# Kernel optimization log

Measured on AMD Instinct MI355X. Metric: run time of the kernel, lower is better.

The kernel has to match this reference:

```python
import jax, jax.numpy as jnp
import numpy as np

P = 16                     # patch size
D = 192                    # embed dim (forced by SAT d_model=192)
NHEAD = 3                  # ViT-Tiny heads
SAT_H, SAT_DK, SAT_DV = 8, 32, 32
N_SLICE = 10
PER_LI = jnp.linspace(0.1, 1.0, N_SLICE)
LN_EPS = 1e-5


def layernorm(z, g, b):
    m = z.mean(-1, keepdims=True)
    v = ((z - m) ** 2).mean(-1, keepdims=True)
    return (z - m) * jax.lax.rsqrt(v + LN_EPS) * g + b


def setup_inputs() -> dict:
    key = jax.random.key(0)
    ks = jax.random.split(key, 32)
    B, IMG, DEPTH, MLP = 128, 224, 12, 4 * D
    S = (IMG // P) ** 2 + 1  # 197 tokens
    n = lambda k, sh: jax.random.normal(k, sh, jnp.float32) * 0.02
    z = lambda sh: jnp.zeros(sh, jnp.float32)
    o = lambda sh: jnp.ones(sh, jnp.float32)
    return {
        "x": jax.random.uniform(ks[0], (B, 3, IMG, IMG), jnp.float32),
        "x_g_norm": jax.random.uniform(ks[1], (B, 1, 56, 56), jnp.float32),
        "patch_w": n(ks[2], (D, 3, P, P)), "patch_b": z((D,)),
        "cls_token": n(ks[3], (1, 1, D)), "pos_embed": n(ks[4], (1, S, D)),
        "eleva_embed": n(ks[5], (1, D)),
        "sat_wq": n(ks[6], (D, SAT_H * SAT_DK)), "sat_bq": z((SAT_H * SAT_DK,)),
        "sat_wk": n(ks[7], (D, SAT_H * SAT_DK)), "sat_bk": z((SAT_H * SAT_DK,)),
        "sat_wv": n(ks[8], (D, SAT_H * SAT_DV)), "sat_bv": z((SAT_H * SAT_DV,)),
        "sat_wo": n(ks[9], (SAT_H * SAT_DV, D)), "sat_bo": z((D,)),
        "ln1_g": o((DEPTH, D)), "ln1_b": z((DEPTH, D)),
        "qkv_w": n(ks[10], (DEPTH, D, 3 * D)), "qkv_b": z((DEPTH, 3 * D)),
        "proj_w": n(ks[11], (DEPTH, D, D)), "proj_b": z((DEPTH, D)),
        "ln2_g": o((DEPTH, D)), "ln2_b": z((DEPTH, D)),
        "fc1_w": n(ks[12], (DEPTH, D, MLP)), "fc1_b": z((DEPTH, MLP)),
        "fc2_w": n(ks[13], (DEPTH, MLP, D)), "fc2_b": z((DEPTH, D)),
        "norm_g": o((D,)), "norm_b": z((D,)),
    }


def _forward(x, x_g_norm, patch_w, patch_b, cls_token, pos_embed, eleva_embed,
             sat_wq, sat_bq, sat_wk, sat_bk, sat_wv, sat_bv, sat_wo, sat_bo,
             ln1_g, ln1_b, qkv_w, qkv_b, proj_w, proj_b, ln2_g, ln2_b,
             fc1_w, fc1_b, fc2_w, fc2_b, norm_g, norm_b):
    B = x.shape[0]
    # --- patch embed: Conv2d(3, D, kernel=P, stride=P) -> [B, N, D] ---
    feat = jax.lax.conv_general_dilated(
        x, patch_w, (P, P), 'VALID', dimension_numbers=('NCHW', 'OIHW', 'NCHW'))
    feat = feat + patch_b[None, :, None, None]
    tokens = feat.reshape(B, D, -1).transpose(0, 2, 1)          # [B, 196, D]
    tok = jnp.concatenate([jnp.broadcast_to(cls_token, (B, 1, D)), tokens], axis=1)
    tok = tok + pos_embed                                        # [B, S, D]
    S = tok.shape[1]
    # --- elevation weight per sample (vectorized bisect + linear interp) ---
    means = x_g_norm.mean(axis=(1, 2, 3))                        # [B]
    idx = jnp.clip(jnp.searchsorted(PER_LI, means, side='left'), 0, N_SLICE - 1)
    per_hi = PER_LI[idx]
    per_lo = jnp.where(idx == 0, 0.0, PER_LI[jnp.maximum(idx - 1, 0)])
    idx_f = idx.astype(jnp.float32)
    idx_inter = idx_f - (per_hi - means) / (per_hi - per_lo)
    w = jnp.where(idx == N_SLICE - 1, idx_f, idx_inter) / N_SLICE  # [B]
    # --- SAT fusion: per (batch, token) a 2-element attention over (token, ele) ---
    ele = jnp.broadcast_to(eleva_embed[0] * w[:, None, None], tok.shape)  # [B,S,D]
    at_in = jnp.stack([tok, ele], axis=2)                        # [B, S, 2, D]
    q = (at_in @ sat_wq + sat_bq).reshape(B, S, 2, SAT_H, SAT_DK)
    k = (at_in @ sat_wk + sat_bk).reshape(B, S, 2, SAT_H, SAT_DK)
    v = (at_in @ sat_wv + sat_bv).reshape(B, S, 2, SAT_H, SAT_DV)
    att = jnp.einsum('bsqhd,bskhd->bshqk', q, k) * (1.0 / np.sqrt(SAT_DK))
    att = jax.nn.softmax(att, axis=-1)
    sat_o = jnp.einsum('bshqk,bskhd->bsqhd', att, v).reshape(B, S, 2, SAT_H * SAT_DV)
    sat_o = sat_o @ sat_wo + sat_bo                              # [B, S, 2, D]
    h = sat_o[..., 0, :] + sat_o[..., 1, :]                      # [B, S, D]
    # --- ViT blocks via scan over stacked layer params ---
    hd = D // NHEAD

    def block(z, p):
        l1g, l1b, qw, qb, pw, pb, l2g, l2b, f1w, f1b, f2w, f2b = p
        y = layernorm(z, l1g, l1b)
        qkv = y @ qw + qb                                        # [B, S, 3D]
        q_, k_, v_ = jnp.split(qkv, 3, axis=-1)
        q_ = q_.reshape(B, S, NHEAD, hd)
        k_ = k_.reshape(B, S, NHEAD, hd)
        v_ = v_.reshape(B, S, NHEAD, hd)
        a = jnp.einsum('bqhd,bkhd->bhqk', q_, k_) * (hd ** -0.5)
        a = jax.nn.softmax(a, axis=-1)
        o = jnp.einsum('bhqk,bkhd->bqhd', a, v_).reshape(B, S, D)
        z = z + o @ pw + pb
        y = layernorm(z, l2g, l2b)
        z = z + jax.nn.gelu(y @ f1w + f1b, approximate=False) @ f2w + f2b
        return z, None

    h, _ = jax.lax.scan(block, h, (ln1_g, ln1_b, qkv_w, qkv_b, proj_w, proj_b,
                                   ln2_g, ln2_b, fc1_w, fc1_b, fc2_w, fc2_b))
    h = layernorm(h, norm_g, norm_b)
    return h[:, 0]                                               # [B, D] cls token


def reference(x, x_g_norm, patch_w, patch_b, cls_token, pos_embed, eleva_embed,
              sat_wq, sat_bq, sat_wk, sat_bk, sat_wv, sat_bv, sat_wo, sat_bo,
              ln1_g, ln1_b, qkv_w, qkv_b, proj_w, proj_b, ln2_g, ln2_b,
              fc1_w, fc1_b, fc2_w, fc2_b, norm_g, norm_b):
    return _forward(x, x_g_norm, patch_w, patch_b, cls_token, pos_embed, eleva_embed,
                    sat_wq, sat_bq, sat_wk, sat_bk, sat_wv, sat_bv, sat_wo, sat_bo,
                    ln1_g, ln1_b, qkv_w, qkv_b, proj_w, proj_b, ln2_g, ln2_b,
                    fc1_w, fc1_b, fc2_w, fc2_b, norm_g, norm_b)
```

## Files before the change

### kernel.cpp

```cpp
#include <hip/hip_runtime.h>


#define BATCH 128
#define SEQ 197
#define BS_ROWS (BATCH * SEQ)
#define DMODEL 192
#define NPATCH 196
#define MROWS_PATCH (BATCH * NPATCH)
#define KPATCH 768
#define MLPDIM 768
#define DEPTH 12
#define SPAD 224

typedef float f32x4 __attribute__((ext_vector_type(4)));
typedef short s16x8 __attribute__((ext_vector_type(8)));

#define AS1 __attribute__((address_space(1)))
#define AS3 __attribute__((address_space(3)))

__device__ __forceinline__ float wredSum(float v) {
#pragma unroll
  for (int o = 32; o > 0; o >>= 1) v += __shfl_xor(v, o, 64);
  return v;
}

__device__ __forceinline__ unsigned short f2bf(float f) {
  union { float f; unsigned u; } v;
  v.f = f;
  unsigned r = v.u + 0x7FFFu + ((v.u >> 16) & 1u);
  return (unsigned short)(r >> 16);
}
__device__ __forceinline__ float bf2f(unsigned short u) {
  union { unsigned u; float f; } v;
  v.u = ((unsigned)u) << 16;
  return v.f;
}

__device__ __forceinline__ int swz(int col, int row) {
  int g8 = col >> 3;
  g8 = (g8 & ~7) | ((g8 & 7) ^ (row & 7));
  return (g8 << 3) | (col & 7);
}

__device__ __forceinline__ float gelu(float x) {
  const float ax = fabsf(x) * 0.70710678118654752f;
  const float t = 1.f / (1.f + 0.3275911f * ax);
  const float y =
      t * (0.254829592f +
           t * (-0.284496736f +
                t * (1.421413741f + t * (-1.453152027f + t * 1.061405429f))));
  const float erfc_ = y * __expf(-ax * ax);
  const float cdf = (x >= 0.f) ? (1.f - 0.5f * erfc_) : (0.5f * erfc_);
  return x * cdf;
}

__global__ __launch_bounds__(256) void eleva_w_kernel(const float* __restrict__ xg,
                                                      float* __restrict__ wout) {
  const int b = blockIdx.x;
  const float* p = xg + (size_t)b * 3136;
  float s = 0.f;
  for (int i = threadIdx.x; i < 3136; i += 256) s += p[i];
  __shared__ float partial[4];
  s = wredSum(s);
  if ((threadIdx.x & 63) == 0) partial[threadIdx.x >> 6] = s;
  __syncthreads();
  if (threadIdx.x == 0) {
    float m = (partial[0] + partial[1] + partial[2] + partial[3]) / 3136.f;
    int idx = 0;
#pragma unroll
    for (int i = 0; i < 10; i++) {
      float pv = 0.1f * (float)(i + 1);
      if (pv < m) idx = i + 1;
    }
    if (idx > 9) idx = 9;
    float wv;
    if (idx == 9) {
      wv = 9.f;
    } else {
      float hi = 0.1f * (float)(idx + 1);
      float lo = (idx == 0) ? 0.f : 0.1f * (float)idx;
      wv = (float)idx - (hi - m) / (hi - lo);
    }
    wout[b] = wv / 10.f;
  }
}

__global__ __launch_bounds__(256) void wprep_kernel(
    const float* __restrict__ qkv_w, const float* __restrict__ proj_w,
    const float* __restrict__ fc1_w, const float* __restrict__ fc2_w,
    const float* __restrict__ satq, const float* __restrict__ satk,
    const float* __restrict__ satv, const float* __restrict__ sato,
    unsigned short* __restrict__ qkv_wt, unsigned short* __restrict__ proj_wt,
    unsigned short* __restrict__ fc1_wt, unsigned short* __restrict__ fc2_wt,
    unsigned short* __restrict__ satqkv_t, unsigned short* __restrict__ sato_t) {
  int bid = blockIdx.x;
  const float* in;
  unsigned short* out;
  int R, C;
  if (bid < 1296) {
    in = qkv_w; out = qkv_wt; R = 192; C = 576;
  } else if ((bid -= 1296) < 432) {
    in = proj_w; out = proj_wt; R = 192; C = 192;
  } else if ((bid -= 432) < 1728) {
    in = fc1_w; out = fc1_wt; R = 192; C = 768;
  } else if ((bid -= 1728) < 1728) {
    in = fc2_w; out = fc2_wt; R = 768; C = 192;
  } else if ((bid -= 1728) < 48) {
    in = satq; out = satqkv_t; R = 192; C = 256;
  } else if ((bid -= 48) < 48) {
    in = satk; out = satqkv_t + 49152; R = 192; C = 256;
  } else if ((bid -= 48) < 48) {
    in = satv; out = satqkv_t + 98304; R = 192; C = 256;
  } else {
    bid -= 48;
    in = sato; out = sato_t; R = 256; C = 192;
  }
  const int tilesX = C >> 5;
  const int tpm = (R >> 5) * tilesX;
  const int mat = bid / tpm;
  const int t_ = bid - mat * tpm;
  const int ty = t_ / tilesX, tx = t_ - ty * tilesX;
  in += (size_t)mat * R * C;
  out += (size_t)mat * R * C;
  const int c0 = tx * 32, r0 = ty * 32;
  __shared__ float t[32][33];
  const int tr = threadIdx.x >> 3, tc = (threadIdx.x & 7) * 4;
  const float4 v = *(const float4*)(in + (size_t)(r0 + tr) * C + c0 + tc);
  t[tr][tc] = v.x; t[tr][tc + 1] = v.y; t[tr][tc + 2] = v.z; t[tr][tc + 3] = v.w;
  __syncthreads();
  ushort4 o;
  o.x = f2bf(t[tc + 0][tr]);
  o.y = f2bf(t[tc + 1][tr]);
  o.z = f2bf(t[tc + 2][tr]);
  o.w = f2bf(t[tc + 3][tr]);
  const int brow = c0 + tr;
  *(ushort4*)(out + (size_t)brow * R + swz(r0 + tc, brow)) = o;
}

__global__ __launch_bounds__(256) void convert_kernel(const float* __restrict__ in,
                                                      unsigned short* __restrict__ out, int n4,
                                                      int K) {
  const int i = blockIdx.x * 256 + threadIdx.x;
  if (i >= n4) return;
  const int flat = i * 4;
  const int row = flat / K, col = flat % K;
  const float4 v = *(const float4*)(in + flat);
  ushort4 o;
  o.x = f2bf(v.x); o.y = f2bf(v.y); o.z = f2bf(v.z); o.w = f2bf(v.w);
  *(ushort4*)(out + (size_t)row * K + swz(col, row)) = o;
}

__global__ __launch_bounds__(256) void im2col_kernel(const float* __restrict__ x,
                                                     unsigned short* __restrict__ col) {
  const int i = blockIdx.x * 256 + threadIdx.x;
  if (i >= MROWS_PATCH * KPATCH / 8) return;
  const int k = (i % 96) * 8, row = i / 96;
  const int b = row / NPATCH, p = row % NPATCH;
  const int py = p / 14, px = p % 14;
  const int c = k >> 8, r = (k >> 4) & 15, cc = k & 15;
  const float* src = x + (((size_t)b * 3 + c) * 224 + (py * 16 + r)) * 224 + (px * 16 + cc);
  const float4 v0 = *(const float4*)src;
  const float4 v1 = *(const float4*)(src + 4);
  s16x8 o;
  o[0] = (short)f2bf(v0.x); o[1] = (short)f2bf(v0.y);
  o[2] = (short)f2bf(v0.z); o[3] = (short)f2bf(v0.w);
  o[4] = (short)f2bf(v1.x); o[5] = (short)f2bf(v1.y);
  o[6] = (short)f2bf(v1.z); o[7] = (short)f2bf(v1.w);
  *(s16x8*)(col + (size_t)row * KPATCH + swz(k, row)) = o;
}

__global__ __launch_bounds__(256) void cls_kernel(const float* __restrict__ cls,
                                                  const float* __restrict__ pos,
                                                  float* __restrict__ H,
                                                  unsigned short* __restrict__ Hbf) {
  const int i = blockIdx.x * 256 + threadIdx.x;
  if (i >= BATCH * DMODEL) return;
  const int b = i / DMODEL, d = i % DMODEL;
  const float v = cls[d] + pos[d];
  const int row = b * SEQ;
  H[(size_t)row * DMODEL + d] = v;
  Hbf[(size_t)row * DMODEL + swz(d, row)] = f2bf(v);
}

__global__ __launch_bounds__(256) void ele_proj_kernel(
    const float* __restrict__ ele_emb, const float* __restrict__ wq, const float* __restrict__ bq,
    const float* __restrict__ wk, const float* __restrict__ bk,
    const float* __restrict__ wv, const float* __restrict__ bv,
    const float* __restrict__ wvec, float* __restrict__ eq, float* __restrict__ ek,
    float* __restrict__ ev, float* __restrict__ satb) {
  const int b = blockIdx.x, t = threadIdx.x;
  if (b == 0) {
    satb[t] = bq[t];
    satb[256 + t] = bk[t];
    satb[512 + t] = bv[t];
  }
  __shared__ float es[DMODEL];
  if (t < DMODEL) es[t] = ele_emb[t] * wvec[b];
  __syncthreads();
  float aq = bq[t], ak = bk[t], av = bv[t];
  for (int d = 0; d < DMODEL; d++) {
    const float e = es[d];
    aq += e * wq[d * 256 + t];
    ak += e * wk[d * 256 + t];
    av += e * wv[d * 256 + t];
  }
  eq[b * 256 + t] = aq;
  ek[b * 256 + t] = ak;
  ev[b * 256 + t] = av;
}

__global__ __launch_bounds__(256) void sat_mix_kernel(
    const unsigned short* __restrict__ qkv768, const float* __restrict__ eq,
    const float* __restrict__ ek, const float* __restrict__ ev,
    unsigned short* __restrict__ o256) {
  const int gid = blockIdx.x * 256 + threadIdx.x;
  const int tok = gid >> 3, h = gid & 7;
  if (tok >= BS_ROWS) return;
  const int b = tok / SEQ;
  const unsigned short* qp = qkv768 + (size_t)tok * 768 + h * 32;
  s16x8 qv[4], kv[4];
#pragma unroll
  for (int i0 = 0; i0 < 4; i0++) {
    qv[i0] = *(const s16x8*)(qp + i0 * 8);
    kv[i0] = *(const s16x8*)(qp + 256 + i0 * 8);
  }
  float eqa[32], eka[32];
  {
    const float4* eqp = (const float4*)(eq + b * 256 + h * 32);
    const float4* ekp = (const float4*)(ek + b * 256 + h * 32);
#pragma unroll
    for (int i0 = 0; i0 < 8; i0++) {
      const float4 a = eqp[i0], c = ekp[i0];
      eqa[i0 * 4] = a.x; eqa[i0 * 4 + 1] = a.y; eqa[i0 * 4 + 2] = a.z; eqa[i0 * 4 + 3] = a.w;
      eka[i0 * 4] = c.x; eka[i0 * 4 + 1] = c.y; eka[i0 * 4 + 2] = c.z; eka[i0 * 4 + 3] = c.w;
    }
  }
  float s00 = 0.f, s01 = 0.f, s10 = 0.f, s11 = 0.f;
#pragma unroll
  for (int d = 0; d < 32; d++) {
    const float q_ = bf2f((unsigned short)qv[d >> 3][d & 7]);
    const float k_ = bf2f((unsigned short)kv[d >> 3][d & 7]);
    s00 += q_ * k_;
    s01 += q_ * eka[d];
    s10 += eqa[d] * k_;
    s11 += eqa[d] * eka[d];
  }
  const float sc = 0.17677669529663687f;
  s00 *= sc; s01 *= sc; s10 *= sc; s11 *= sc;
  const float m0 = fmaxf(s00, s01), m1 = fmaxf(s10, s11);
  const float e00 = __expf(s00 - m0), e01 = __expf(s01 - m0);
  const float e10 = __expf(s10 - m1), e11 = __expf(s11 - m1);
  const float w0 = e00 / (e00 + e01) + e10 / (e10 + e11);
  const float w1 = e01 / (e00 + e01) + e11 / (e10 + e11);
  unsigned short* op = o256 + (size_t)tok * 256;
  const float4* evp = (const float4*)(ev + b * 256 + h * 32);
#pragma unroll
  for (int i0 = 0; i0 < 4; i0++) {
    const s16x8 vv = *(const s16x8*)(qp + 512 + i0 * 8);
    const float4 e0 = evp[i0 * 2], e1 = evp[i0 * 2 + 1];
    float ev8[8] = {e0.x, e0.y, e0.z, e0.w, e1.x, e1.y, e1.z, e1.w};
    s16x8 o;
#pragma unroll
    for (int e = 0; e < 8; e++)
      o[e] = (short)f2bf(w0 * bf2f((unsigned short)vv[e]) + w1 * ev8[e]);
    *(s16x8*)(op + swz(h * 32 + i0 * 8, tok)) = o;
  }
}

template <int EPI, bool SWZO, int BN, int BM>
__global__ __launch_bounds__(256, 4)
void gemm_mfma(const unsigned short* __restrict__ A,
               const unsigned short* __restrict__ Bt,
               const float* __restrict__ bias,
               const float* __restrict__ res,
               void* __restrict__ Cout,
               unsigned short* __restrict__ aux_hbf,
               const float* __restrict__ aux_pos,
               const float* __restrict__ lng,
               const float* __restrict__ lnb,
               int M, int N, int K, int nx) {
  constexpr int NJ = 3;
  constexpr int MI = (BM == 128) ? 4 : 2;
  constexpr bool LNF = (EPI == 5 || EPI == 6);
  constexpr int LNROWS = LNF ? BM : 1;
  int mt, nt;
  if (BM == 128) {
    const int bid = blockIdx.x;
    const int e = bid & 7, i = bid >> 3;
    nt = i % nx;
    mt = e + 8 * (i / nx);
    if (mt * BM >= M) return;
  } else {
    mt = blockIdx.y;
    nt = blockIdx.x;
  }
  __shared__ unsigned short As[BM * 64];
  __shared__ unsigned short Bs[BN * 64];
  __shared__ float2 lnbuf[4][LNROWS];
  const int tid = threadIdx.x, lane = tid & 63, w = tid >> 6;
  const int n0 = nt * BN;
  const int m0 = mt * BM;
  const int c = lane & 15, g = lane >> 4;
  const int wm = (BM == 128) ? (w >> 1) * 64 : 0;
  const int wn = (BM == 128) ? (w & 1) * 96 / 2 : w * 48;
  f32x4 acc[MI][NJ] = {};

  const int ar = (lane >> 3);
  const int acol = (lane & 7) * 8;

  for (int k0 = 0; k0 < K; k0 += 64) {
#pragma unroll
    for (int it = 0; it < BM / 32; it++) {
      const int r = w * (BM / 4) + it * 8 + ar;
      const unsigned short* gp = A + (size_t)(m0 + r) * K + k0 + acol;
      __builtin_amdgcn_global_load_lds(
          (const AS1 unsigned int*)gp,
          (AS3 unsigned int*)(As + (w * (BM / 4) + it * 8) * 64), 16, 0, 0);
    }
#pragma unroll
    for (int it = 0; it < BN / 32; it++) {
      const int r = w * (BN / 4) + it * 8 + ar;
      const unsigned short* gp = Bt + (size_t)(n0 + r) * K + k0 + acol;
      __builtin_amdgcn_global_load_lds(
          (const AS1 unsigned int*)gp,
          (AS3 unsigned int*)(Bs + (w * (BN / 4) + it * 8) * 64), 16, 0, 0);
    }
    __syncthreads();
#pragma unroll
    for (int kk = 0; kk < 2; kk++) {
      const int sw = (((kk * 4 + g) ^ (c & 7))) << 3;
      s16x8 af[MI], bfr[NJ];
#pragma unroll
      for (int i = 0; i < MI; i++)
        af[i] = *(const s16x8*)&As[(wm + i * 16 + c) * 64 + sw];
#pragma unroll
      for (int j = 0; j < NJ; j++)
        bfr[j] = *(const s16x8*)&Bs[(wn + j * 16 + c) * 64 + sw];
#pragma unroll
      for (int i = 0; i < MI; i++)
#pragma unroll
        for (int j = 0; j < NJ; j++)
          acc[i][j] = __builtin_amdgcn_mfma_f32_16x16x32_bf16(af[i], bfr[j], acc[i][j], 0, 0, 0);
    }
    __syncthreads();
  }

  const int ncol0 = n0 + wn + c;
  float bv[NJ];
#pragma unroll
  for (int j = 0; j < NJ; j++) bv[j] = bias[ncol0 + j * 16] * (EPI == 6 ? 2.f : 1.f);

  if constexpr (LNF) {
#pragma unroll
    for (int i = 0; i < MI; i++) {
#pragma unroll
      for (int r_ = 0; r_ < 4; r_++) {
        const int lr = wm + i * 16 + g * 4 + r_;
        const int mrow = m0 + lr;
        float s1 = 0.f, s2 = 0.f;
#pragma unroll
        for (int j = 0; j < NJ; j++) {
          float v = acc[i][j][r_] + bv[j];
          if (EPI == 5) v += res[(size_t)mrow * DMODEL + ncol0 + j * 16];
          acc[i][j][r_] = v;
          ((float*)Cout)[(size_t)mrow * DMODEL + ncol0 + j * 16] = v;
          s1 += v;
          s2 += v * v;
        }
#pragma unroll
        for (int o = 1; o <= 8; o <<= 1) {
          s1 += __shfl_xor(s1, o, 64);
          s2 += __shfl_xor(s2, o, 64);
        }
        if (c == 0) lnbuf[w][lr] = make_float2(s1, s2);
      }
    }
    __syncthreads();
    float lg[NJ], lb[NJ];
#pragma unroll
    for (int j = 0; j < NJ; j++) { lg[j] = lng[ncol0 + j * 16]; lb[j] = lnb[ncol0 + j * 16]; }
#pragma unroll
    for (int i = 0; i < MI; i++) {
#pragma unroll
      for (int r_ = 0; r_ < 4; r_++) {
        const int lr = wm + i * 16 + g * 4 + r_;
        const int mrow = m0 + lr;
        const float2 a0 = lnbuf[0][lr], a1 = lnbuf[1][lr];
        const float2 a2 = lnbuf[2][lr], a3 = lnbuf[3][lr];
        const float mean = (a0.x + a1.x + a2.x + a3.x) * (1.f / 192.f);
        const float var = (a0.y + a1.y + a2.y + a3.y) * (1.f / 192.f) - mean * mean;
        const float inv = rsqrtf(var + 1e-5f);
#pragma unroll
        for (int j = 0; j < NJ; j++) {
          const int col = ncol0 + j * 16;
          const float yn = (acc[i][j][r_] - mean) * inv * lg[j] + lb[j];
          aux_hbf[(size_t)mrow * DMODEL + swz(col, mrow)] = f2bf(yn);
        }
      }
    }
  } else if (EPI == 7 && n0 >= 384) {
#pragma unroll
    for (int i = 0; i < MI; i++) {
#pragma unroll
      for (int r_ = 0; r_ < 4; r_++) {
        const int mrow = m0 + wm + i * 16 + g * 4 + r_;
        const int b = mrow / SEQ;
        const int s = mrow - b * SEQ;
#pragma unroll
        for (int j = 0; j < NJ; j++) {
          const int vcol = ncol0 + j * 16 - 384;
          const int h = vcol >> 6, d = vcol & 63;
          aux_hbf[((size_t)((b * 3 + h) * 64 + d)) * SPAD + s] = f2bf(acc[i][j][r_] + bv[j]);
        }
      }
    }
  } else {
#pragma unroll
    for (int i = 0; i < MI; i++) {
#pragma unroll
      for (int r_ = 0; r_ < 4; r_++) {
        const int mrow = m0 + wm + i * 16 + g * 4 + r_;
        if (EPI == 4) {
          const int bb = mrow / 196;
          const int p = mrow - bb * 196;
          const int drow = mrow + bb + 1;
#pragma unroll
          for (int j = 0; j < NJ; j++) {
            const int col = ncol0 + j * 16;
            const float v = acc[i][j][r_] + bv[j] + aux_pos[(size_t)(p + 1) * DMODEL + col];
            ((float*)Cout)[(size_t)drow * DMODEL + col] = v;
            aux_hbf[(size_t)drow * DMODEL + swz(col, drow)] = f2bf(v);
          }
        } else {
#pragma unroll
          for (int j = 0; j < NJ; j++) {
            float v = acc[i][j][r_] + bv[j];
            const int col = ncol0 + j * 16;
            const size_t rowoff = (size_t)mrow * N;
            ((unsigned short*)Cout)[rowoff + (SWZO ? swz(col, mrow) : col)] = f2bf(v);
          }
        }
      }
    }
  }
}

__global__ __launch_bounds__(256, 2)
void mlp_fused_kernel(const unsigned short* __restrict__ Yin,
                      const unsigned short* __restrict__ w1,
                      const unsigned short* __restrict__ w2,
                      const float* __restrict__ b1,
                      const float* __restrict__ b2,
                      float* __restrict__ H,
                      unsigned short* __restrict__ Yout,
                      const float* __restrict__ lng,
                      const float* __restrict__ lnb) {
  __shared__ unsigned short Abuf[32 * 192];
  __shared__ unsigned short W1buf[64 * 192];
  __shared__ unsigned short W2buf[192 * 64];
  __shared__ unsigned short Pbuf[2][32 * 64];
  __shared__ float2 lnbuf[4][32];
  const int tid = threadIdx.x, lane = tid & 63, w = tid >> 6;
  const int c = lane & 15, g = lane >> 4;
  const int m0 = blockIdx.x * 32;

#pragma unroll
  for (int it = 0; it < 3; it++) {
    const int flat = w * 192 + it * 64 + lane;
    const int r = flat / 24, s = flat - r * 24;
    const unsigned short* gp = Yin + (size_t)(m0 + r) * DMODEL + s * 8;
    __builtin_amdgcn_global_load_lds((const AS1 unsigned int*)gp,
                                     (AS3 unsigned int*)(Abuf + flat * 8), 16, 0, 0);
  }
  auto stageW1 = [&](int ch) {
#pragma unroll
    for (int it = 0; it < 6; it++) {
      const int flat = w * 384 + it * 64 + lane;
      const int r = flat / 24, s = flat - r * 24;
      const unsigned short* gp = w1 + (size_t)(ch * 64 + r) * DMODEL + s * 8;
      __builtin_amdgcn_global_load_lds((const AS1 unsigned int*)gp,
                                       (AS3 unsigned int*)(W1buf + flat * 8), 16, 0, 0);
    }
  };
  auto stageW2 = [&](int ch) {
#pragma unroll
    for (int it = 0; it < 6; it++) {
      const int flat = w * 384 + it * 64 + lane;
      const int r = flat >> 3, s = flat & 7;
      const unsigned short* gp = w2 + (size_t)r * MLPDIM + ch * 64 + s * 8;
      __builtin_amdgcn_global_load_lds((const AS1 unsigned int*)gp,
                                       (AS3 unsigned int*)(W2buf + flat * 8), 16, 0, 0);
    }
  };
  stageW1(0);
  stageW2(0);
  __syncthreads();

  f32x4 acc2[2][3] = {};
  for (int ch = 0; ch < 12; ++ch) {
    const float bb1 = b1[ch * 64 + w * 16 + c];
    f32x4 a1[2] = {};
#pragma unroll
    for (int kk = 0; kk < 6; kk++) {
      const int slot = kk * 4 + g;
      const int sw1 = ((slot & ~7) | ((slot & 7) ^ (c & 7))) << 3;
      const s16x8 bf1 = *(const s16x8*)&W1buf[(w * 16 + c) * DMODEL + sw1];
#pragma unroll
      for (int i = 0; i < 2; i++) {
        const s16x8 af = *(const s16x8*)&Abuf[(i * 16 + c) * DMODEL + sw1];
        a1[i] = __builtin_amdgcn_mfma_f32_16x16x32_bf16(af, bf1, a1[i], 0, 0, 0);
      }
    }
    unsigned short* P = &Pbuf[ch & 1][0];
#pragma unroll
    for (int i = 0; i < 2; i++) {
#pragma unroll
      for (int r_ = 0; r_ < 4; r_++) {
        const int row = i * 16 + g * 4 + r_;
        const int col = w * 16 + c;
        const int slotp = (col >> 3) ^ (row & 7);
        P[row * 64 + slotp * 8 + (col & 7)] = f2bf(gelu(a1[i][r_] + bb1));
      }
    }
    __syncthreads();
    if (ch < 11) stageW1(ch + 1);
#pragma unroll
    for (int kk = 0; kk < 2; kk++) {
      const int slot = kk * 4 + g;
      const int sw2 = (slot ^ (c & 7)) << 3;
      s16x8 af2[2], bf2[3];
#pragma unroll
      for (int i = 0; i < 2; i++) af2[i] = *(const s16x8*)&P[(i * 16 + c) * 64 + sw2];
#pragma unroll
      for (int j = 0; j < 3; j++)
        bf2[j] = *(const s16x8*)&W2buf[(w * 48 + j * 16 + c) * 64 + sw2];
#pragma unroll
      for (int i = 0; i < 2; i++)
#pragma unroll
        for (int j = 0; j < 3; j++)
          acc2[i][j] = __builtin_amdgcn_mfma_f32_16x16x32_bf16(af2[i], bf2[j], acc2[i][j], 0, 0, 0);
    }
    __syncthreads();
    if (ch < 11) stageW2(ch + 1);
  }

  const int ncol0 = w * 48 + c;
  float bv[3];
#pragma unroll
  for (int j = 0; j < 3; j++) bv[j] = b2[ncol0 + j * 16];
#pragma unroll
  for (int i = 0; i < 2; i++) {
#pragma unroll
    for (int r_ = 0; r_ < 4; r_++) {
      const int lr = i * 16 + g * 4 + r_;
      const int mrow = m0 + lr;
      float s1 = 0.f, s2 = 0.f;
#pragma unroll
      for (int j = 0; j < 3; j++) {
        float v = acc2[i][j][r_] + bv[j] + H[(size_t)mrow * DMODEL + ncol0 + j * 16];
        acc2[i][j][r_] = v;
        H[(size_t)mrow * DMODEL + ncol0 + j * 16] = v;
        s1 += v;
        s2 += v * v;
      }
#pragma unroll
      for (int o = 1; o <= 8; o <<= 1) {
        s1 += __shfl_xor(s1, o, 64);
        s2 += __shfl_xor(s2, o, 64);
      }
      if (c == 0) lnbuf[w][lr] = make_float2(s1, s2);
    }
  }
  __syncthreads();
  float lg[3], lb[3];
#pragma unroll
  for (int j = 0; j < 3; j++) { lg[j] = lng[ncol0 + j * 16]; lb[j] = lnb[ncol0 + j * 16]; }
#pragma unroll
  for (int i = 0; i < 2; i++) {
#pragma unroll
    for (int r_ = 0; r_ < 4; r_++) {
      const int lr = i * 16 + g * 4 + r_;
      const int mrow = m0 + lr;
      const float2 a0 = lnbuf[0][lr], a1 = lnbuf[1][lr];
      const float2 a2 = lnbuf[2][lr], a3 = lnbuf[3][lr];
      const float mean = (a0.x + a1.x + a2.x + a3.x) * (1.f / 192.f);
      const float var = (a0.y + a1.y + a2.y + a3.y) * (1.f / 192.f) - mean * mean;
      const float inv = rsqrtf(var + 1e-5f);
#pragma unroll
      for (int j = 0; j < 3; j++) {
        const int col = ncol0 + j * 16;
        const float yn = (acc2[i][j][r_] - mean) * inv * lg[j] + lb[j];
        Yout[(size_t)mrow * DMODEL + swz(col, mrow)] = f2bf(yn);
      }
    }
  }
}

__global__ __launch_bounds__(256) void final_ln_kernel(const float* __restrict__ H,
                                                       const float* __restrict__ g,
                                                       const float* __restrict__ bta,
                                                       float* __restrict__ out) {
  const int w = threadIdx.x >> 6, lane = threadIdx.x & 63;
  const int bi = blockIdx.x * 4 + w;
  if (bi >= BATCH) return;
  const float* x = H + (size_t)bi * SEQ * DMODEL;
  const float x0 = x[lane], x1 = x[lane + 64], x2 = x[lane + 128];
  const float m = wredSum(x0 + x1 + x2) * (1.f / 192.f);
  const float d0 = x0 - m, d1 = x1 - m, d2 = x2 - m;
  const float v = wredSum(d0 * d0 + d1 * d1 + d2 * d2) * (1.f / 192.f);
  const float inv = rsqrtf(v + 1e-5f);
  float* y = out + (size_t)bi * DMODEL;
  y[lane] = d0 * inv * g[lane] + bta[lane];
  y[lane + 64] = d1 * inv * g[lane + 64] + bta[lane + 64];
  y[lane + 128] = d2 * inv * g[lane + 128] + bta[lane + 128];
}

__global__ __launch_bounds__(64) void attn_mfma_kernel(const unsigned short* __restrict__ qkv,
                                                       const unsigned short* __restrict__ vt,
                                                       unsigned short* __restrict__ out) {
  const int bid = blockIdx.x;
  const int bh = bid / 13, qt = bid % 13;
  const int b = bh / 3, h = bh % 3;
  const int row0 = b * SEQ;
  const int q0 = qt * 16;
  const int lane = threadIdx.x;
  const int c = lane & 15, g = lane >> 4;

  __shared__ __attribute__((aligned(16))) unsigned short P[16][232];

  const int qr = row0 + min(q0 + c, SEQ - 1);
  const unsigned short* qp = qkv + (size_t)qr * 576 + h * 64 + g * 8;
  const s16x8 qlo = *(const s16x8*)qp;
  const s16x8 qhi = *(const s16x8*)(qp + 32);

  f32x4 acc[13];
#pragma unroll
  for (int t = 0; t < 13; t++) {
    const int kr = row0 + min(t * 16 + c, SEQ - 1);
    const unsigned short* kp = qkv + (size_t)kr * 576 + 192 + h * 64 + g * 8;
    const s16x8 klo = *(const s16x8*)kp;
    const s16x8 khi = *(const s16x8*)(kp + 32);
    f32x4 z = {0.f, 0.f, 0.f, 0.f};
    z = __builtin_amdgcn_mfma_f32_16x16x32_bf16(qlo, klo, z, 0, 0, 0);
    acc[t] = __builtin_amdgcn_mfma_f32_16x16x32_bf16(qhi, khi, z, 0, 0, 0);
  }

  const bool m12 = (c >= 5);
#pragma unroll
  for (int r = 0; r < 4; r++) {
    float mx = -INFINITY;
#pragma unroll
    for (int t = 0; t < 13; t++) {
      const float v = (t == 12 && m12) ? -INFINITY : acc[t][r];
      mx = fmaxf(mx, v);
    }
#pragma unroll
    for (int o = 1; o <= 8; o <<= 1) mx = fmaxf(mx, __shfl_xor(mx, o, 64));
    const float ms = mx * 0.125f;
    float sum = 0.f;
#pragma unroll
    for (int t = 0; t < 13; t++) {
      const float e = (t == 12 && m12) ? 0.f : __expf(acc[t][r] * 0.125f - ms);
      acc[t][r] = e;
      sum += e;
    }
#pragma unroll
    for (int o = 1; o <= 8; o <<= 1) sum += __shfl_xor(sum, o, 64);
    const float inv = 1.f / sum;
#pragma unroll
    for (int t = 0; t < 13; t++) P[g * 4 + r][t * 16 + c] = f2bf(acc[t][r] * inv);
  }
  {
    unsigned short z4[4] = {0, 0, 0, 0};
    *(uint2*)&P[c][208 + g * 4] = *(uint2*)z4;
  }
  __builtin_amdgcn_s_waitcnt(0);

  f32x4 oacc[4];
#pragma unroll
  for (int dt = 0; dt < 4; dt++) oacc[dt] = (f32x4){0.f, 0.f, 0.f, 0.f};
  const unsigned short* vbase = vt + (size_t)bh * 64 * SPAD;
#pragma unroll
  for (int ch = 0; ch < 7; ch++) {
    const s16x8 pa = *(const s16x8*)&P[c][ch * 32 + g * 8];
#pragma unroll
    for (int dt = 0; dt < 4; dt++) {
      const s16x8 vb = *(const s16x8*)(vbase + (size_t)(dt * 16 + c) * SPAD + ch * 32 + g * 8);
      oacc[dt] = __builtin_amdgcn_mfma_f32_16x16x32_bf16(pa, vb, oacc[dt], 0, 0, 0);
    }
  }

#pragma unroll
  for (int dt = 0; dt < 4; dt++) {
#pragma unroll
    for (int r = 0; r < 4; r++) {
      const int q = q0 + g * 4 + r;
      if (q < SEQ) {
        const int trow = row0 + q;
        out[(size_t)trow * DMODEL + swz(h * 64 + dt * 16 + c, trow)] = f2bf(oacc[dt][r]);
      }
    }
  }
}

extern "C" void kernel_launch(void* const* d_in, const int* in_sizes, int n_in,
                              void* d_out, int out_size, void* d_ws, size_t ws_size,
                              hipStream_t stream) {
  const float* x       = (const float*)d_in[0];
  const float* xg      = (const float*)d_in[1];
  const float* patch_w = (const float*)d_in[2];
  const float* patch_b = (const float*)d_in[3];
  const float* cls_tok = (const float*)d_in[4];
  const float* pos_emb = (const float*)d_in[5];
  const float* ele_emb = (const float*)d_in[6];
  const float* sat_wq  = (const float*)d_in[7];
  const float* sat_bq  = (const float*)d_in[8];
  const float* sat_wk  = (const float*)d_in[9];
  const float* sat_bk  = (const float*)d_in[10];
  const float* sat_wv  = (const float*)d_in[11];
  const float* sat_bv  = (const float*)d_in[12];
  const float* sat_wo  = (const float*)d_in[13];
  const float* sat_bo  = (const float*)d_in[14];
  const float* ln1_g   = (const float*)d_in[15];
  const float* ln1_b   = (const float*)d_in[16];
  const float* qkv_w   = (const float*)d_in[17];
  const float* qkv_b   = (const float*)d_in[18];
  const float* proj_w  = (const float*)d_in[19];
  const float* proj_b  = (const float*)d_in[20];
  const float* ln2_g   = (const float*)d_in[21];
  const float* ln2_b   = (const float*)d_in[22];
  const float* fc1_w   = (const float*)d_in[23];
  const float* fc1_b   = (const float*)d_in[24];
  const float* fc2_w   = (const float*)d_in[25];
  const float* fc2_b   = (const float*)d_in[26];
  const float* norm_g  = (const float*)d_in[27];
  const float* norm_b  = (const float*)d_in[28];
  float* out = (float*)d_out;
  float* ws = (float*)d_ws;

  float* W_ELE = ws;
  float* EQ = ws + 256;
  float* EK = EQ + 32768;
  float* EV = EK + 32768;
  float* H = ws + 98560;
  unsigned short* Hbf   = (unsigned short*)(ws + 4940032);
  unsigned short* Ybf   = (unsigned short*)(ws + 7360768);
  unsigned short* QKVbf = (unsigned short*)(ws + 9781504);
  unsigned short* MLPbf = (unsigned short*)(ws + 17043712);
  unsigned short* VTB   = (unsigned short*)(ws + 26726656);
  unsigned short* WTS   = (unsigned short*)(ws + 29479168);
  float* SATB = ws + 32305408;
  unsigned short* ATTNbf = (unsigned short*)(ws + 32306176);

  unsigned short* qkv_wt   = WTS;
  unsigned short* proj_wt  = WTS + 1327104;
  unsigned short* fc1_wt   = WTS + 1769472;
  unsigned short* fc2_wt   = WTS + 3538944;
  unsigned short* patch_bf = WTS + 5308416;
  unsigned short* satqkv_t = WTS + 5455872;
  unsigned short* sato_t   = WTS + 5603328;

  unsigned short* COLbf   = MLPbf;
  unsigned short* SATQKV  = MLPbf;
  unsigned short* O256bf  = QKVbf;

  hipMemsetAsync(VTB, 0, (size_t)BATCH * 3 * 64 * SPAD * 2, stream);

  wprep_kernel<<<5376, 256, 0, stream>>>(qkv_w, proj_w, fc1_w, fc2_w, sat_wq, sat_wk,
                                         sat_wv, sat_wo, qkv_wt, proj_wt, fc1_wt, fc2_wt,
                                         satqkv_t, sato_t);
  convert_kernel<<<144, 256, 0, stream>>>(patch_w, patch_bf, 36864, KPATCH);

  eleva_w_kernel<<<BATCH, 256, 0, stream>>>(xg, W_ELE);

  im2col_kernel<<<(MROWS_PATCH * KPATCH / 8) / 256, 256, 0, stream>>>(x, COLbf);
  gemm_mfma<4, false, 96, 128><<<400, 256, 0, stream>>>(
      COLbf, patch_bf, patch_b, nullptr, H, Hbf, pos_emb, nullptr, nullptr,
      MROWS_PATCH, DMODEL, KPATCH, 2);
  cls_kernel<<<(BATCH * DMODEL) / 256, 256, 0, stream>>>(cls_tok, pos_emb, H, Hbf);

  ele_proj_kernel<<<BATCH, 256, 0, stream>>>(ele_emb, sat_wq, sat_bq, sat_wk, sat_bk,
                                             sat_wv, sat_bv, W_ELE, EQ, EK, EV, SATB);
  gemm_mfma<0, false, 96, 128><<<1600, 256, 0, stream>>>(
      Hbf, satqkv_t, SATB, nullptr, SATQKV, nullptr, nullptr, nullptr, nullptr,
      BS_ROWS, 768, DMODEL, 8);
  sat_mix_kernel<<<BS_ROWS / 32, 256, 0, stream>>>(SATQKV, EQ, EK, EV, O256bf);
  gemm_mfma<6, false, 192, 32><<<dim3(1, 788), 256, 0, stream>>>(
      O256bf, sato_t, sat_bo, nullptr, H, Ybf, nullptr, ln1_g, ln1_b,
      BS_ROWS, DMODEL, 256, 1);

  for (int l = 0; l < DEPTH; l++) {
    gemm_mfma<7, false, 96, 128><<<1200, 256, 0, stream>>>(
        Ybf, qkv_wt + (size_t)l * 110592, qkv_b + l * 576, nullptr, QKVbf, VTB, nullptr,
        nullptr, nullptr, BS_ROWS, 576, DMODEL, 6);
    attn_mfma_kernel<<<BATCH * 3 * 13, 64, 0, stream>>>(QKVbf, VTB, ATTNbf);
    gemm_mfma<5, false, 192, 32><<<dim3(1, 788), 256, 0, stream>>>(
        ATTNbf, proj_wt + (size_t)l * 36864, proj_b + l * DMODEL, H, H, Ybf, nullptr,
        ln2_g + l * DMODEL, ln2_b + l * DMODEL, BS_ROWS, DMODEL, DMODEL, 1);
    const float* nlg = (l < DEPTH - 1) ? (ln1_g + (l + 1) * DMODEL) : norm_g;
    const float* nlb = (l < DEPTH - 1) ? (ln1_b + (l + 1) * DMODEL) : norm_b;
    mlp_fused_kernel<<<788, 256, 0, stream>>>(
        Ybf, fc1_wt + (size_t)l * 147456, fc2_wt + (size_t)l * 147456,
        fc1_b + l * MLPDIM, fc2_b + l * DMODEL, H, Ybf, nlg, nlb);
  }

  final_ln_kernel<<<BATCH / 4, 256, 0, stream>>>(H, norm_g, norm_b, out);
}
```

Baseline: 1.736 ms.

## Load GEMM operands directly into registers for LN-fused projections and MLP

Splits the 32-row LayerNorm-fused GEMM path into a dedicated ln_gemm kernel that reads A and weight fragments straight from global memory into registers, with no LDS staging or block barriers in the K loop. The fused MLP kernel is reworked the same way: activations and W1/W2 fragments are loaded per lane into registers, and only the small intermediate P tile stays in shared memory. The aim is to cut LDS footprint and barrier overhead and raise occupancy, relying on L2/L1 to serve the shared weights. The risk is more redundant global loads and exposed load latency, since nothing is prefetched into LDS ahead of the MFMAs.

```diff
diff --git a/kernel.cpp b/kernel.cpp
--- a/kernel.cpp
+++ b/kernel.cpp
@@ -267,42 +267,29 @@
   }
 }
 
-template <int EPI, bool SWZO, int BN, int BM>
+template <int EPI>
 __global__ __launch_bounds__(256, 4)
 void gemm_mfma(const unsigned short* __restrict__ A,
                const unsigned short* __restrict__ Bt,
                const float* __restrict__ bias,
-               const float* __restrict__ res,
                void* __restrict__ Cout,
                unsigned short* __restrict__ aux_hbf,
                const float* __restrict__ aux_pos,
-               const float* __restrict__ lng,
-               const float* __restrict__ lnb,
                int M, int N, int K, int nx) {
   constexpr int NJ = 3;
-  constexpr int MI = (BM == 128) ? 4 : 2;
-  constexpr bool LNF = (EPI == 5 || EPI == 6);
-  constexpr int LNROWS = LNF ? BM : 1;
-  int mt, nt;
-  if (BM == 128) {
-    const int bid = blockIdx.x;
-    const int e = bid & 7, i = bid >> 3;
-    nt = i % nx;
-    mt = e + 8 * (i / nx);
-    if (mt * BM >= M) return;
-  } else {
-    mt = blockIdx.y;
-    nt = blockIdx.x;
-  }
-  __shared__ unsigned short As[BM * 64];
-  __shared__ unsigned short Bs[BN * 64];
-  __shared__ float2 lnbuf[4][LNROWS];
+  constexpr int MI = 4;
+  const int bid = blockIdx.x;
+  const int e = bid & 7, i_ = bid >> 3;
+  const int nt = i_ % nx;
+  const int mt = e + 8 * (i_ / nx);
+  if (mt * 128 >= M) return;
+  __shared__ unsigned short As[128 * 64];
+  __shared__ unsigned short Bs[96 * 64];
   const int tid = threadIdx.x, lane = tid & 63, w = tid >> 6;
-  const int n0 = nt * BN;
-  const int m0 = mt * BM;
+  const int n0 = nt * 96;
+  const int m0 = mt * 128;
   const int c = lane & 15, g = lane >> 4;
-  const int wm = (BM == 128) ? (w >> 1) * 64 : 0;
-  const int wn = (BM == 128) ? (w & 1) * 96 / 2 : w * 48;
+  const int wm = (w >> 1) * 64, wn = (w & 1) * 48;
   f32x4 acc[MI][NJ] = {};
 
   const int ar = (lane >> 3);
@@ -310,20 +297,20 @@
 
   for (int k0 = 0; k0 < K; k0 += 64) {
 #pragma unroll
-    for (int it = 0; it < BM / 32; it++) {
-      const int r = w * (BM / 4) + it * 8 + ar;
+    for (int it = 0; it < 4; it++) {
+      const int r = w * 32 + it * 8 + ar;
       const unsigned short* gp = A + (size_t)(m0 + r) * K + k0 + acol;
       __builtin_amdgcn_global_load_lds(
           (const AS1 unsigned int*)gp,
-          (AS3 unsigned int*)(As + (w * (BM / 4) + it * 8) * 64), 16, 0, 0);
-    }
-#pragma unroll
-    for (int it = 0; it < BN / 32; it++) {
-      const int r = w * (BN / 4) + it * 8 + ar;
+          (AS3 unsigned int*)(As + (w * 32 + it * 8) * 64), 16, 0, 0);
+    }
+#pragma unroll
+    for (int it = 0; it < 3; it++) {
+      const int r = w * 24 + it * 8 + ar;
       const unsigned short* gp = Bt + (size_t)(n0 + r) * K + k0 + acol;
       __builtin_amdgcn_global_load_lds(
           (const AS1 unsigned int*)gp,
-          (AS3 unsigned int*)(Bs + (w * (BN / 4) + it * 8) * 64), 16, 0, 0);
+          (AS3 unsigned int*)(Bs + (w * 24 + it * 8) * 64), 16, 0, 0);
     }
     __syncthreads();
 #pragma unroll
@@ -348,57 +335,9 @@
   const int ncol0 = n0 + wn + c;
   float bv[NJ];
 #pragma unroll
-  for (int j = 0; j < NJ; j++) bv[j] = bias[ncol0 + j * 16] * (EPI == 6 ? 2.f : 1.f);
-
-  if constexpr (LNF) {
-#pragma unroll
-    for (int i = 0; i < MI; i++) {
-#pragma unroll
-      for (int r_ = 0; r_ < 4; r_++) {
-        const int lr = wm + i * 16 + g * 4 + r_;
-        const int mrow = m0 + lr;
-        float s1 = 0.f, s2 = 0.f;
-#pragma unroll
-        for (int j = 0; j < NJ; j++) {
-          float v = acc[i][j][r_] + bv[j];
-          if (EPI == 5) v += res[(size_t)mrow * DMODEL + ncol0 + j * 16];
-          acc[i][j][r_] = v;
-          ((float*)Cout)[(size_t)mrow * DMODEL + ncol0 + j * 16] = v;
-          s1 += v;
-          s2 += v * v;
-        }
-#pragma unroll
-        for (int o = 1; o <= 8; o <<= 1) {
-          s1 += __shfl_xor(s1, o, 64);
-          s2 += __shfl_xor(s2, o, 64);
-        }
-        if (c == 0) lnbuf[w][lr] = make_float2(s1, s2);
-      }
-    }
-    __syncthreads();
-    float lg[NJ], lb[NJ];
-#pragma unroll
-    for (int j = 0; j < NJ; j++) { lg[j] = lng[ncol0 + j * 16]; lb[j] = lnb[ncol0 + j * 16]; }
-#pragma unroll
-    for (int i = 0; i < MI; i++) {
-#pragma unroll
-      for (int r_ = 0; r_ < 4; r_++) {
-        const int lr = wm + i * 16 + g * 4 + r_;
-        const int mrow = m0 + lr;
-        const float2 a0 = lnbuf[0][lr], a1 = lnbuf[1][lr];
-        const float2 a2 = lnbuf[2][lr], a3 = lnbuf[3][lr];
-        const float mean = (a0.x + a1.x + a2.x + a3.x) * (1.f / 192.f);
-        const float var = (a0.y + a1.y + a2.y + a3.y) * (1.f / 192.f) - mean * mean;
-        const float inv = rsqrtf(var + 1e-5f);
-#pragma unroll
-        for (int j = 0; j < NJ; j++) {
-          const int col = ncol0 + j * 16;
-          const float yn = (acc[i][j][r_] - mean) * inv * lg[j] + lb[j];
-          aux_hbf[(size_t)mrow * DMODEL + swz(col, mrow)] = f2bf(yn);
-        }
-      }
-    }
-  } else if (EPI == 7 && n0 >= 384) {
+  for (int j = 0; j < NJ; j++) bv[j] = bias[ncol0 + j * 16];
+
+  if (EPI == 7 && n0 >= 384) {
 #pragma unroll
     for (int i = 0; i < MI; i++) {
 #pragma unroll
@@ -434,10 +373,9 @@
         } else {
 #pragma unroll
           for (int j = 0; j < NJ; j++) {
-            float v = acc[i][j][r_] + bv[j];
+            const float v = acc[i][j][r_] + bv[j];
             const int col = ncol0 + j * 16;
-            const size_t rowoff = (size_t)mrow * N;
-            ((unsigned short*)Cout)[rowoff + (SWZO ? swz(col, mrow) : col)] = f2bf(v);
+            ((unsigned short*)Cout)[(size_t)mrow * N + col] = f2bf(v);
           }
         }
       }
@@ -445,7 +383,95 @@
   }
 }
 
-__global__ __launch_bounds__(256, 2)
+template <int EPI, int K>
+__global__ __launch_bounds__(256)
+void ln_gemm(const unsigned short* __restrict__ A,
+             const unsigned short* __restrict__ Bt,
+             const float* __restrict__ bias,
+             float* __restrict__ H,
+             unsigned short* __restrict__ Yout,
+             const float* __restrict__ lng,
+             const float* __restrict__ lnb) {
+  __shared__ float2 lnbuf[4][32];
+  const int tid = threadIdx.x, lane = tid & 63, w = tid >> 6;
+  const int c = lane & 15, g = lane >> 4;
+  const int cx = c & 7;
+  const int m0 = blockIdx.x * 32;
+  const int wn = w * 48;
+  f32x4 acc[2][3] = {};
+#pragma unroll
+  for (int ks = 0; ks < K / 32; ks++) {
+    const int s = ks * 4 + g;
+    const int ss = (s & ~7) | ((s & 7) ^ cx);
+    s16x8 af[2], bfr[3];
+#pragma unroll
+    for (int i = 0; i < 2; i++)
+      af[i] = *(const s16x8*)(A + (size_t)(m0 + i * 16 + c) * K + ss * 8);
+#pragma unroll
+    for (int j = 0; j < 3; j++)
+      bfr[j] = *(const s16x8*)(Bt + (size_t)(wn + j * 16 + c) * K + ss * 8);
+#pragma unroll
+    for (int i = 0; i < 2; i++)
+#pragma unroll
+      for (int j = 0; j < 3; j++)
+        acc[i][j] = __builtin_amdgcn_mfma_f32_16x16x32_bf16(af[i], bfr[j], acc[i][j], 0, 0, 0);
+  }
+
+  const int ncol0 = wn + c;
+  float bv[3];
+#pragma unroll
+  for (int j = 0; j < 3; j++) bv[j] = bias[ncol0 + j * 16] * (EPI == 6 ? 2.f : 1.f);
+
+#pragma unroll
+  for (int i = 0; i < 2; i++) {
+#pragma unroll
+    for (int r_ = 0; r_ < 4; r_++) {
+      const int lr = i * 16 + g * 4 + r_;
+      const int mrow = m0 + lr;
+      float s1 = 0.f, s2 = 0.f;
+#pragma unroll
+      for (int j = 0; j < 3; j++) {
+        float v = acc[i][j][r_] + bv[j];
+        if (EPI == 5) v += H[(size_t)mrow * DMODEL + ncol0 + j * 16];
+        acc[i][j][r_] = v;
+        H[(size_t)mrow * DMODEL + ncol0 + j * 16] = v;
+        s1 += v;
+        s2 += v * v;
+      }
+#pragma unroll
+      for (int o = 1; o <= 8; o <<= 1) {
+        s1 += __shfl_xor(s1, o, 64);
+        s2 += __shfl_xor(s2, o, 64);
+      }
+      if (c == 0) lnbuf[w][lr] = make_float2(s1, s2);
+    }
+  }
+  __syncthreads();
+  float lg[3], lb[3];
+#pragma unroll
+  for (int j = 0; j < 3; j++) { lg[j] = lng[ncol0 + j * 16]; lb[j] = lnb[ncol0 + j * 16]; }
+#pragma unroll
+  for (int i = 0; i < 2; i++) {
+#pragma unroll
+    for (int r_ = 0; r_ < 4; r_++) {
+      const int lr = i * 16 + g * 4 + r_;
+      const int mrow = m0 + lr;
+      const float2 a0 = lnbuf[0][lr], a1 = lnbuf[1][lr];
+      const float2 a2 = lnbuf[2][lr], a3 = lnbuf[3][lr];
+      const float mean = (a0.x + a1.x + a2.x + a3.x) * (1.f / 192.f);
+      const float var = (a0.y + a1.y + a2.y + a3.y) * (1.f / 192.f) - mean * mean;
+      const float inv = rsqrtf(var + 1e-5f);
+#pragma unroll
+      for (int j = 0; j < 3; j++) {
+        const int col = ncol0 + j * 16;
+        const float yn = (acc[i][j][r_] - mean) * inv * lg[j] + lb[j];
+        Yout[(size_t)mrow * DMODEL + swz(col, mrow)] = f2bf(yn);
+      }
+    }
+  }
+}
+
+__global__ __launch_bounds__(256)
 void mlp_fused_kernel(const unsigned short* __restrict__ Yin,
                       const unsigned short* __restrict__ w1,
                       const unsigned short* __restrict__ w2,
@@ -455,63 +481,45 @@
                       unsigned short* __restrict__ Yout,
                       const float* __restrict__ lng,
                       const float* __restrict__ lnb) {
-  __shared__ unsigned short Abuf[32 * 192];
-  __shared__ unsigned short W1buf[64 * 192];
-  __shared__ unsigned short W2buf[192 * 64];
-  __shared__ unsigned short Pbuf[2][32 * 64];
+  __shared__ unsigned short P[32 * 64];
   __shared__ float2 lnbuf[4][32];
   const int tid = threadIdx.x, lane = tid & 63, w = tid >> 6;
   const int c = lane & 15, g = lane >> 4;
+  const int cx = c & 7;
   const int m0 = blockIdx.x * 32;
 
-#pragma unroll
-  for (int it = 0; it < 3; it++) {
-    const int flat = w * 192 + it * 64 + lane;
-    const int r = flat / 24, s = flat - r * 24;
-    const unsigned short* gp = Yin + (size_t)(m0 + r) * DMODEL + s * 8;
-    __builtin_amdgcn_global_load_lds((const AS1 unsigned int*)gp,
-                                     (AS3 unsigned int*)(Abuf + flat * 8), 16, 0, 0);
-  }
-  auto stageW1 = [&](int ch) {
-#pragma unroll
-    for (int it = 0; it < 6; it++) {
-      const int flat = w * 384 + it * 64 + lane;
-      const int r = flat / 24, s = flat - r * 24;
-      const unsigned short* gp = w1 + (size_t)(ch * 64 + r) * DMODEL + s * 8;
-      __builtin_amdgcn_global_load_lds((const AS1 unsigned int*)gp,
-                                       (AS3 unsigned int*)(W1buf + flat * 8), 16, 0, 0);
-    }
-  };
-  auto stageW2 = [&](int ch) {
-#pragma unroll
-    for (int it = 0; it < 6; it++) {
-      const int flat = w * 384 + it * 64 + lane;
-      const int r = flat >> 3, s = flat & 7;
-      const unsigned short* gp = w2 + (size_t)r * MLPDIM + ch * 64 + s * 8;
-      __builtin_amdgcn_global_load_lds((const AS1 unsigned int*)gp,
-                                       (AS3 unsigned int*)(W2buf + flat * 8), 16, 0, 0);
-    }
-  };
-  stageW1(0);
-  stageW2(0);
-  __syncthreads();
+  s16x8 afA0[6], afA1[6];
+#pragma unroll
+  for (int kk = 0; kk < 6; kk++) {
+    const int s = kk * 4 + g;
+    const int ss = (s & ~7) | ((s & 7) ^ cx);
+    afA0[kk] = *(const s16x8*)(Yin + (size_t)(m0 + c) * DMODEL + ss * 8);
+    afA1[kk] = *(const s16x8*)(Yin + (size_t)(m0 + 16 + c) * DMODEL + ss * 8);
+  }
 
   f32x4 acc2[2][3] = {};
   for (int ch = 0; ch < 12; ++ch) {
+    s16x8 w1f[6];
+#pragma unroll
+    for (int kk = 0; kk < 6; kk++) {
+      const int s = kk * 4 + g;
+      const int ss = (s & ~7) | ((s & 7) ^ cx);
+      w1f[kk] = *(const s16x8*)(w1 + (size_t)(ch * 64 + w * 16 + c) * DMODEL + ss * 8);
+    }
+    s16x8 w2f[2][3];
+#pragma unroll
+    for (int kk = 0; kk < 2; kk++)
+#pragma unroll
+      for (int j = 0; j < 3; j++)
+        w2f[kk][j] = *(const s16x8*)(w2 + (size_t)(w * 48 + j * 16 + c) * MLPDIM +
+                                     (ch * 8 + ((kk * 4 + g) ^ cx)) * 8);
+    f32x4 a1[2] = {};
+#pragma unroll
+    for (int kk = 0; kk < 6; kk++) {
+      a1[0] = __builtin_amdgcn_mfma_f32_16x16x32_bf16(afA0[kk], w1f[kk], a1[0], 0, 0, 0);
+      a1[1] = __builtin_amdgcn_mfma_f32_16x16x32_bf16(afA1[kk], w1f[kk], a1[1], 0, 0, 0);
+    }
     const float bb1 = b1[ch * 64 + w * 16 + c];
-    f32x4 a1[2] = {};
-#pragma unroll
-    for (int kk = 0; kk < 6; kk++) {
-      const int slot = kk * 4 + g;
-      const int sw1 = ((slot & ~7) | ((slot & 7) ^ (c & 7))) << 3;
-      const s16x8 bf1 = *(const s16x8*)&W1buf[(w * 16 + c) * DMODEL + sw1];
-#pragma unroll
-      for (int i = 0; i < 2; i++) {
-        const s16x8 af = *(const s16x8*)&Abuf[(i * 16 + c) * DMODEL + sw1];
-        a1[i] = __builtin_amdgcn_mfma_f32_16x16x32_bf16(af, bf1, a1[i], 0, 0, 0);
-      }
-    }
-    unsigned short* P = &Pbuf[ch & 1][0];
 #pragma unroll
     for (int i = 0; i < 2; i++) {
 #pragma unroll
@@ -523,25 +531,19 @@
       }
     }
     __syncthreads();
-    if (ch < 11) stageW1(ch + 1);
 #pragma unroll
     for (int kk = 0; kk < 2; kk++) {
-      const int slot = kk * 4 + g;
-      const int sw2 = (slot ^ (c & 7)) << 3;
-      s16x8 af2[2], bf2[3];
+      const int sw2 = ((kk * 4 + g) ^ cx) << 3;
+      s16x8 af2[2];
 #pragma unroll
       for (int i = 0; i < 2; i++) af2[i] = *(const s16x8*)&P[(i * 16 + c) * 64 + sw2];
 #pragma unroll
-      for (int j = 0; j < 3; j++)
-        bf2[j] = *(const s16x8*)&W2buf[(w * 48 + j * 16 + c) * 64 + sw2];
-#pragma unroll
       for (int i = 0; i < 2; i++)
 #pragma unroll
         for (int j = 0; j < 3; j++)
-          acc2[i][j] = __builtin_amdgcn_mfma_f32_16x16x32_bf16(af2[i], bf2[j], acc2[i][j], 0, 0, 0);
+          acc2[i][j] = __builtin_amdgcn_mfma_f32_16x16x32_bf16(af2[i], w2f[kk][j], acc2[i][j], 0, 0, 0);
     }
     __syncthreads();
-    if (ch < 11) stageW2(ch + 1);
   }
 
   const int ncol0 = w * 48 + c;
@@ -774,29 +776,25 @@
   eleva_w_kernel<<<BATCH, 256, 0, stream>>>(xg, W_ELE);
 
   im2col_kernel<<<(MROWS_PATCH * KPATCH / 8) / 256, 256, 0, stream>>>(x, COLbf);
-  gemm_mfma<4, false, 96, 128><<<400, 256, 0, stream>>>(
-      COLbf, patch_bf, patch_b, nullptr, H, Hbf, pos_emb, nullptr, nullptr,
-      MROWS_PATCH, DMODEL, KPATCH, 2);
+  gemm_mfma<4><<<400, 256, 0, stream>>>(COLbf, patch_bf, patch_b, H, Hbf, pos_emb,
+                                        MROWS_PATCH, DMODEL, KPATCH, 2);
   cls_kernel<<<(BATCH * DMODEL) / 256, 256, 0, stream>>>(cls_tok, pos_emb, H, Hbf);
 
   ele_proj_kernel<<<BATCH, 256, 0, stream>>>(ele_emb, sat_wq, sat_bq, sat_wk, sat_bk,
                                              sat_wv, sat_bv, W_ELE, EQ, EK, EV, SATB);
-  gemm_mfma<0, false, 96, 128><<<1600, 256, 0, stream>>>(
-      Hbf, satqkv_t, SATB, nullptr, SATQKV, nullptr, nullptr, nullptr, nullptr,
-      BS_ROWS, 768, DMODEL, 8);
+  gemm_mfma<0><<<1600, 256, 0, stream>>>(Hbf, satqkv_t, SATB, SATQKV, nullptr, nullptr,
+                                         BS_ROWS, 768, DMODEL, 8);
   sat_mix_kernel<<<BS_ROWS / 32, 256, 0, stream>>>(SATQKV, EQ, EK, EV, O256bf);
-  gemm_mfma<6, false, 192, 32><<<dim3(1, 788), 256, 0, stream>>>(
-      O256bf, sato_t, sat_bo, nullptr, H, Ybf, nullptr, ln1_g, ln1_b,
-      BS_ROWS, DMODEL, 256, 1);
+  ln_gemm<6, 256><<<788, 256, 0, stream>>>(O256bf, sato_t, sat_bo, H, Ybf, ln1_g, ln1_b);
 
   for (int l = 0; l < DEPTH; l++) {
-    gemm_mfma<7, false, 96, 128><<<1200, 256, 0, stream>>>(
-        Ybf, qkv_wt + (size_t)l * 110592, qkv_b + l * 576, nullptr, QKVbf, VTB, nullptr,
-        nullptr, nullptr, BS_ROWS, 576, DMODEL, 6);
+    gemm_mfma<7><<<1200, 256, 0, stream>>>(Ybf, qkv_wt + (size_t)l * 110592,
+                                           qkv_b + l * 576, QKVbf, VTB, nullptr,
+                                           BS_ROWS, 576, DMODEL, 6);
     attn_mfma_kernel<<<BATCH * 3 * 13, 64, 0, stream>>>(QKVbf, VTB, ATTNbf);
-    gemm_mfma<5, false, 192, 32><<<dim3(1, 788), 256, 0, stream>>>(
-        ATTNbf, proj_wt + (size_t)l * 36864, proj_b + l * DMODEL, H, H, Ybf, nullptr,
-        ln2_g + l * DMODEL, ln2_b + l * DMODEL, BS_ROWS, DMODEL, DMODEL, 1);
+    ln_gemm<5, 192><<<788, 256, 0, stream>>>(ATTNbf, proj_wt + (size_t)l * 36864,
+                                             proj_b + l * DMODEL, H, Ybf,
+                                             ln2_g + l * DMODEL, ln2_b + l * DMODEL);
     const float* nlg = (l < DEPTH - 1) ? (ln1_g + (l + 1) * DMODEL) : norm_g;
     const float* nlb = (l < DEPTH - 1) ? (ln1_b + (l + 1) * DMODEL) : norm_b;
     mlp_fused_kernel<<<788, 256, 0, stream>>>(
```

New measurement: 1.832 ms. 5.5% more time.
